# Performance work log

Hardware: AMD Instinct MI355X
Metric: run time of the kernel (lower is better)

The kernel has to match this reference:

```python
import jax, jax.numpy as jnp
import numpy as np

N_NODES = 50000
N_EDGES = 800000
N_GRAPHS = 500
NEG_SLOPE = 0.2
BN_EPS = 1e-5


def gat_layer(x, src, dst, W, al, ar, b):
    # x: [N, F_in]; W: [F_in, H*D]; al/ar: [H, D]; b: [H*D]
    H, D = al.shape
    feat = (x @ W).reshape(N_NODES, H, D)          # [N,H,D]
    el = jnp.sum(feat * al, axis=-1)               # [N,H] src-side score
    er = jnp.sum(feat * ar, axis=-1)               # [N,H] dst-side score
    e = el[src] + er[dst]                          # [E,H]
    e = jnp.where(e > 0, e, NEG_SLOPE * e)         # leaky_relu(0.2)
    # edge softmax over incoming edges of each dst node
    m = jax.ops.segment_max(e, dst, num_segments=N_NODES)       # [N,H]
    ex = jnp.exp(e - m[dst])                                    # [E,H]
    denom = jax.ops.segment_sum(ex, dst, num_segments=N_NODES)  # [N,H]
    alpha = ex / denom[dst]                                     # [E,H]
    # weighted scatter-aggregation of source features
    msg = feat[src] * alpha[:, :, None]                          # [E,H,D]
    out = jax.ops.segment_sum(msg, dst, num_segments=N_NODES)    # [N,H,D]
    return out + b.reshape(H, D)


def batch_norm(x, gamma, beta):
    # training-mode BN over node dimension (biased variance, as torch)
    mu = jnp.mean(x, axis=0)
    var = jnp.mean((x - mu) ** 2, axis=0)
    return gamma * (x - mu) * jax.lax.rsqrt(var + BN_EPS) + beta


def setup_inputs() -> dict:
    key = jax.random.key(0)
    ks = jax.random.split(key, 20)
    s = lambda shape, k, scale=0.05: jax.random.normal(ks[k], shape, jnp.float32) * scale
    return {
        "x": jax.random.normal(ks[0], (N_NODES, 128), jnp.float32),
        "edge_src": jax.random.randint(ks[1], (N_EDGES,), 0, N_NODES),
        "edge_dst": jax.random.randint(ks[2], (N_EDGES,), 0, N_NODES),
        "graph_ids": jax.random.randint(ks[3], (N_NODES,), 0, N_GRAPHS),
        "W0": s((128, 128), 4), "al0": s((4, 32), 5), "ar0": s((4, 32), 6), "b0": jnp.zeros((128,), jnp.float32),
        "W1": s((128, 128), 7), "al1": s((4, 32), 8), "ar1": s((4, 32), 9), "b1": jnp.zeros((128,), jnp.float32),
        "W2": s((128, 32), 10), "al2": s((1, 32), 11), "ar2": s((1, 32), 12), "b2": jnp.zeros((32,), jnp.float32),
        "g0": jnp.ones((128,), jnp.float32), "beta0": jnp.zeros((128,), jnp.float32),
        "g1": jnp.ones((128,), jnp.float32), "beta1": jnp.zeros((128,), jnp.float32),
        "Wc": s((32, 10), 13), "bc": jnp.zeros((10,), jnp.float32),
    }


def reference(x, edge_src, edge_dst, graph_ids,
              W0, al0, ar0, b0, W1, al1, ar1, b1, W2, al2, ar2, b2,
              g0, beta0, g1, beta1, Wc, bc):
    # layer 0: GAT -> flatten heads -> BN -> ReLU (dropout = identity in eval)
    h = gat_layer(x, edge_src, edge_dst, W0, al0, ar0, b0).reshape(N_NODES, -1)
    h = jax.nn.relu(batch_norm(h, g0, beta0))
    # layer 1
    h = gat_layer(h, edge_src, edge_dst, W1, al1, ar1, b1).reshape(N_NODES, -1)
    h = jax.nn.relu(batch_norm(h, g1, beta1))
    # layer 2 (single head) -> squeeze head dim
    h = gat_layer(h, edge_src, edge_dst, W2, al2, ar2, b2)[:, 0, :]  # [N, 32]
    # sum pooling per graph
    hg = jax.ops.segment_sum(h, graph_ids, num_segments=N_GRAPHS)    # [G, 32]
    return hg @ Wc + bc                                              # [G, 10]
```

## Files before the change

kernel.cpp:

```cpp
#include <hip/hip_runtime.h>
#include <math.h>

#define NNODES 50000
#define NEDGES 800000
#define NGRAPHS 500
#define NEG_SLOPE 0.2f
#define BN_EPS 1e-5f
#define NRANGE 196
#define RH_EPB 4096
#define RH_NB ((NEDGES + RH_EPB - 1) / RH_EPB)
#define MAXRE 5120
#define BN_NB 200
#define BN_RPB 250

typedef unsigned int uint;
typedef unsigned short ushort;
typedef __attribute__((ext_vector_type(8))) short bf16x8;
typedef __attribute__((ext_vector_type(4))) float f32x4;

__device__ __forceinline__ float bf2f(ushort u) { return __uint_as_float(((uint)u) << 16); }
__device__ __forceinline__ float bflo(uint u)   { return __uint_as_float(u << 16); }
__device__ __forceinline__ float bfhi(uint u)   { return __uint_as_float(u & 0xffff0000u); }
__device__ __forceinline__ ushort f2bf(float f) {
    uint u = __float_as_uint(f);
    u = (u + 0x7fffu + ((u >> 16) & 1u)) >> 16;
    return (ushort)u;
}

__device__ __forceinline__ float ld_dev(const float* p) {
    return __hip_atomic_load(p, __ATOMIC_RELAXED, __HIP_MEMORY_SCOPE_AGENT);
}
__device__ __forceinline__ void st_dev(float* p, float v) {
    __hip_atomic_store(p, v, __ATOMIC_RELAXED, __HIP_MEMORY_SCOPE_AGENT);
}

__global__ __launch_bounds__(256) void prep_hist_kernel(
        const float* __restrict__ W0, const float* __restrict__ W1,
        const float* __restrict__ W2, ushort* __restrict__ Wt0,
        ushort* __restrict__ Wt1, ushort* __restrict__ Wt2,
        const int* __restrict__ dst, int* __restrict__ rhist,
        int* __restrict__ rowptr) {
    int t = blockIdx.x * 256 + threadIdx.x;
    if (t == 0) rowptr[NNODES] = NEDGES;
    if (t < 16384) {
        int k = t >> 7, m = t & 127;
        Wt0[m * 128 + k] = f2bf(W0[t]);
    } else if (t < 32768) {
        int i = t - 16384;
        int k = i >> 7, m = i & 127;
        Wt1[m * 128 + k] = f2bf(W1[i]);
    } else if (t < 36864) {
        int i = t - 32768;
        int k = i >> 5, m = i & 31;
        Wt2[m * 128 + k] = f2bf(W2[i]);
    }
    __shared__ int cnt[NRANGE];
    for (int i = threadIdx.x; i < NRANGE; i += 256) cnt[i] = 0;
    __syncthreads();
    int base = blockIdx.x * RH_EPB;
    int end = base + RH_EPB; if (end > NEDGES) end = NEDGES;
    for (int i = base + threadIdx.x; i < end; i += 256) atomicAdd(&cnt[dst[i] >> 8], 1);
    __syncthreads();
    for (int i = threadIdx.x; i < NRANGE; i += 256)
        if (cnt[i]) atomicAdd(&rhist[i], cnt[i]);
}

__global__ __launch_bounds__(256) void reorder_kernel(
        const int* __restrict__ src, const int* __restrict__ dst,
        const int* __restrict__ rhist, int* __restrict__ rcursor,
        uint* __restrict__ bucket) {
    __shared__ int cnt[NRANGE];
    __shared__ int bofs[NRANGE];
    __shared__ int rb[256];
    const int t = threadIdx.x;
    rb[t] = (t < NRANGE) ? rhist[t] : 0;
    if (t < NRANGE) cnt[t] = 0;
    __syncthreads();
    for (int off = 1; off < 256; off <<= 1) {
        int u = (t >= off) ? rb[t - off] : 0;
        __syncthreads();
        rb[t] += u;
        __syncthreads();
    }
    int base = blockIdx.x * RH_EPB;
    int end = base + RH_EPB; if (end > NEDGES) end = NEDGES;
    for (int i = base + t; i < end; i += 256) atomicAdd(&cnt[dst[i] >> 8], 1);
    __syncthreads();
    for (int i = t; i < NRANGE; i += 256) {
        int c = cnt[i];
        int ex = (i == 0) ? 0 : rb[i - 1];
        bofs[i] = c ? (ex + atomicAdd(&rcursor[i], c)) : 0;
    }
    __syncthreads();
    for (int i = t; i < NRANGE; i += 256) cnt[i] = 0;
    __syncthreads();
    for (int i = base + t; i < end; i += 256) {
        int d = dst[i], r = d >> 8;
        int loc = atomicAdd(&cnt[r], 1);
        bucket[bofs[r] + loc] = (uint)src[i] | ((uint)(d & 255) << 16);
    }
}

__global__ __launch_bounds__(256) void range_csr_kernel(const int* __restrict__ rhist,
                                                        const uint* __restrict__ bucket,
                                                        int* __restrict__ rowptr,
                                                        int* __restrict__ csr_src) {
    __shared__ uint ebuf[MAXRE];
    __shared__ int deg[256], excl[256], cur[256];
    __shared__ int rb[256];
    const int r = blockIdx.x;
    const int t = threadIdx.x;
    rb[t] = (t < NRANGE) ? rhist[t] : 0;
    __syncthreads();
    for (int off = 1; off < 256; off <<= 1) {
        int u = (t >= off) ? rb[t - off] : 0;
        __syncthreads();
        rb[t] += u;
        __syncthreads();
    }
    const int b0 = (r == 0) ? 0 : rb[r - 1];
    const int cnt = rb[r] - b0;
    deg[t] = 0; cur[t] = 0;
    __syncthreads();
    for (int i = t; i < cnt; i += 256) {
        uint e = bucket[b0 + i];
        ebuf[i] = e;
        atomicAdd(&deg[e >> 16], 1);
    }
    __syncthreads();
    excl[t] = deg[t];
    __syncthreads();
    for (int off = 1; off < 256; off <<= 1) {
        int u = (t >= off) ? excl[t - off] : 0;
        __syncthreads();
        excl[t] += u;
        __syncthreads();
    }
    int myExcl = (t == 0) ? 0 : excl[t - 1];
    __syncthreads();
    excl[t] = myExcl;
    __syncthreads();
    int node = r * 256 + t;
    if (node < NNODES) rowptr[node] = b0 + myExcl;
    for (int i = t; i < cnt; i += 256) {
        uint e = ebuf[i];
        int dl = e >> 16;
        int loc = atomicAdd(&cur[dl], 1);
        csr_src[b0 + excl[dl] + loc] = (int)(e & 0xffffu);
    }
}

template <int M, bool HASBN>
__global__ __launch_bounds__(256) void gemm_mfma_kernel(
        const void* __restrict__ Xv, const ushort* __restrict__ Wt,
        const float* __restrict__ scale, const float* __restrict__ shift,
        const float* __restrict__ al, const float* __restrict__ ar,
        ushort* __restrict__ Y, float* __restrict__ el, float* __restrict__ er, int N) {
    constexpr int H   = M / 32;
    constexpr int BR  = (M == 128) ? 64 : 128;
    constexpr int RT  = (M == 128) ? 4 : 2;
    constexpr int CT  = 2;
    constexpr int LDK = 136;
    __shared__ ushort xs[BR][LDK];
    __shared__ ushort ws[M][LDK];
    __shared__ float scs[128], shs[128];

    const int tid = threadIdx.x, wv = tid >> 6, lane = tid & 63;
    const int rowBase = blockIdx.x * BR;

    if (HASBN) {
        if (tid < 128) {
            scs[tid] = scale[tid];
            shs[tid] = shift[tid];
        }
        __syncthreads();
    }

    if (HASBN) {
        const ushort* X = (const ushort*)Xv;
        for (int i = tid; i < BR * 16; i += 256) {
            int rr = i >> 4, q = i & 15;
            int gr = rowBase + rr;
            uint4 u = make_uint4(0, 0, 0, 0);
            if (gr < N) u = *(const uint4*)(X + (size_t)gr * 128 + q * 8);
            uint arr[4] = {u.x, u.y, u.z, u.w};
            ushort* o = &xs[rr][q * 8];
#pragma unroll
            for (int j = 0; j < 4; ++j) {
                int c = q * 8 + j * 2;
                float lo = fmaxf(bflo(arr[j]) * scs[c] + shs[c], 0.f);
                float hi = fmaxf(bfhi(arr[j]) * scs[c + 1] + shs[c + 1], 0.f);
                o[j * 2]     = f2bf(lo);
                o[j * 2 + 1] = f2bf(hi);
            }
        }
    } else {
        const float* X = (const float*)Xv;
        for (int i = tid; i < BR * 32; i += 256) {
            int rr = i >> 5, c4 = i & 31;
            int gr = rowBase + rr;
            float4 v = make_float4(0.f, 0.f, 0.f, 0.f);
            if (gr < N) v = *(const float4*)(X + (size_t)gr * 128 + c4 * 4);
            ushort* o = &xs[rr][c4 * 4];
            o[0] = f2bf(v.x); o[1] = f2bf(v.y); o[2] = f2bf(v.z); o[3] = f2bf(v.w);
        }
    }
    for (int i = tid; i < M * 16; i += 256) {
        int rr = i >> 4, kc = (i & 15) * 8;
        *(uint4*)&ws[rr][kc] = *(const uint4*)(Wt + rr * 128 + kc);
    }
    __syncthreads();

    const int waveRow = (M == 128) ? 0 : (wv * 32);
    const int waveCol = (M == 128) ? (wv * 32) : 0;
    const int fr = lane & 15, quad = lane >> 4;

    f32x4 acc[RT][CT];
#pragma unroll
    for (int rt = 0; rt < RT; ++rt)
#pragma unroll
        for (int ct = 0; ct < CT; ++ct) acc[rt][ct] = (f32x4){0.f, 0.f, 0.f, 0.f};

#pragma unroll
    for (int ks = 0; ks < 4; ++ks) {
        const int kb = ks * 32 + quad * 8;
        bf16x8 a[RT], b[CT];
#pragma unroll
        for (int rt = 0; rt < RT; ++rt) a[rt] = *(const bf16x8*)&xs[waveRow + rt * 16 + fr][kb];
#pragma unroll
        for (int ct = 0; ct < CT; ++ct) b[ct] = *(const bf16x8*)&ws[waveCol + ct * 16 + fr][kb];
#pragma unroll
        for (int rt = 0; rt < RT; ++rt)
#pragma unroll
            for (int ct = 0; ct < CT; ++ct)
                acc[rt][ct] = __builtin_amdgcn_mfma_f32_16x16x32_bf16(a[rt], b[ct], acc[rt][ct], 0, 0, 0);
    }

#pragma unroll
    for (int rt = 0; rt < RT; ++rt)
#pragma unroll
        for (int ct = 0; ct < CT; ++ct)
#pragma unroll
            for (int rg = 0; rg < 4; ++rg) {
                int gr = rowBase + waveRow + rt * 16 + quad * 4 + rg;
                int gc = waveCol + ct * 16 + fr;
                if (gr < N) Y[(size_t)gr * M + gc] = f2bf(acc[rt][ct][rg]);
            }

    const float a0 = al[waveCol + fr],      a1 = al[waveCol + 16 + fr];
    const float g0 = ar[waveCol + fr],      g1 = ar[waveCol + 16 + fr];
    const int h = (M == 128) ? wv : 0;
#pragma unroll
    for (int rt = 0; rt < RT; ++rt)
#pragma unroll
        for (int rg = 0; rg < 4; ++rg) {
            float pe = acc[rt][0][rg] * a0 + acc[rt][1][rg] * a1;
            float pr = acc[rt][0][rg] * g0 + acc[rt][1][rg] * g1;
#pragma unroll
            for (int off = 1; off < 16; off <<= 1) {
                pe += __shfl_xor(pe, off);
                pr += __shfl_xor(pr, off);
            }
            int grow = rowBase + waveRow + rt * 16 + quad * 4 + rg;
            if (fr == 0 && grow < N) {
                el[grow * H + h] = pe;
                er[grow * H + h] = pr;
            }
        }
}

__global__ __launch_bounds__(256) void gat_gather4_kernel(
        const int* __restrict__ rowptr, const int* __restrict__ csr_src,
        const float* __restrict__ el, const float* __restrict__ er,
        const ushort* __restrict__ feat, const float* __restrict__ bias,
        ushort* __restrict__ xnext) {
    const int d = __builtin_amdgcn_readfirstlane(
        (int)((blockIdx.x * blockDim.x + threadIdx.x) >> 6));
    const int lane = threadIdx.x & 63;
    if (d >= NNODES) return;
    const int h   = lane >> 4;
    const int k   = lane & 15;
    const int grp = lane & 48;
    const int c0  = lane * 2;
    const int r0 = rowptr[d];
    const int deg = rowptr[d + 1] - r0;
    const float erh = er[d * 4 + h];
    float dnm = 0.f, ax = 0.f, ay = 0.f;

    for (int j0 = 0; j0 < deg; j0 += 16) {
        int eidx = j0 + k;
        int s_e = 0;
        float ex = 0.f;
        if (eidx < deg) {
            s_e = csr_src[r0 + eidx];
            float v = el[s_e * 4 + h] + erh;
            v = v > 0.f ? v : NEG_SLOPE * v;
            ex = __expf(v);
        }
        dnm += ex;
        uint u[16];
#pragma unroll
        for (int jj = 0; jj < 16; ++jj) {
            int sj = __builtin_amdgcn_readlane(s_e, jj);
            u[jj] = *(const uint*)(feat + (size_t)sj * 128 + c0);
        }
#pragma unroll
        for (int jj = 0; jj < 16; ++jj) {
            float exj = __shfl(ex, grp + jj);
            ax = fmaf(exj, bflo(u[jj]), ax);
            ay = fmaf(exj, bfhi(u[jj]), ay);
        }
    }
#pragma unroll
    for (int off = 1; off < 16; off <<= 1) dnm += __shfl_xor(dnm, off);
    float inv = (dnm > 0.f) ? 1.f / dnm : 0.f;
    float vx = ax * inv + bias[c0];
    float vy = ay * inv + bias[c0 + 1];
    uint pk = ((uint)f2bf(vy) << 16) | (uint)f2bf(vx);
    *(uint*)(xnext + (size_t)d * 128 + c0) = pk;
}

__global__ __launch_bounds__(256) void bn_stats_kernel(
        const ushort* __restrict__ X, float* __restrict__ psum, float* __restrict__ psumsq,
        const float* __restrict__ g, const float* __restrict__ beta,
        float* __restrict__ scale, float* __restrict__ shift, int* __restrict__ counter) {
    const uint* X32 = (const uint*)X;
    int uc = threadIdx.x & 63;
    int rq = threadIdx.x >> 6;
    int r0 = blockIdx.x * BN_RPB;
    float s0 = 0.f, s1 = 0.f, ss0 = 0.f, ss1 = 0.f;
    for (int r = r0 + rq; r < r0 + BN_RPB; r += 4) {
        uint u = X32[(size_t)r * 64 + uc];
        float lo = bflo(u), hi = bfhi(u);
        s0 += lo; ss0 += lo * lo;
        s1 += hi; ss1 += hi * hi;
    }
    __shared__ float red[4][256], redsq[4][256];
    red[rq][uc * 2] = s0;      red[rq][uc * 2 + 1] = s1;
    redsq[rq][uc * 2] = ss0;   redsq[rq][uc * 2 + 1] = ss1;
    __syncthreads();
    int t = threadIdx.x;
    if (t < 128) {
        st_dev(&psum[blockIdx.x * 128 + t], red[0][t] + red[1][t] + red[2][t] + red[3][t]);
    } else {
        int c = t - 128;
        st_dev(&psumsq[blockIdx.x * 128 + c], redsq[0][c] + redsq[1][c] + redsq[2][c] + redsq[3][c]);
    }
    __syncthreads();
    __shared__ int isLast;
    if (t == 0) isLast = (atomicAdd(counter, 1) == (int)gridDim.x - 1);
    __syncthreads();
    if (!isLast) return;
    __threadfence();
    if (t < 128) {
        float s = 0.f, ss = 0.f;
        for (int b = 0; b < BN_NB; ++b) {
            s += ld_dev(&psum[b * 128 + t]);
            ss += ld_dev(&psumsq[b * 128 + t]);
        }
        const float inv = 1.f / NNODES;
        float mu = s * inv;
        float var = ss * inv - mu * mu;
        float sc = g[t] * rsqrtf(var + BN_EPS);
        scale[t] = sc;
        shift[t] = beta[t] - mu * sc;
    }
}

__global__ __launch_bounds__(256) void gat_gather1_kernel(
        const int* __restrict__ rowptr, const int* __restrict__ csr_src,
        const float* __restrict__ el, const float* __restrict__ er,
        const ushort* __restrict__ feat, const float* __restrict__ bias,
        const int* __restrict__ gid, float* __restrict__ pooled) {
    const int d = __builtin_amdgcn_readfirstlane(
        (int)((blockIdx.x * blockDim.x + threadIdx.x) >> 6));
    int lane = threadIdx.x & 63;
    if (d >= NNODES) return;
    const int r0 = rowptr[d];
    const int deg = rowptr[d + 1] - r0;
    const int half = lane >> 5;
    const int c    = lane & 31;
    const float erh = er[d];
    float dnm = 0.f, acc = 0.f;

    for (int j0 = 0; j0 < deg; j0 += 32) {
        int eidx = j0 + (lane & 31);
        int s_e = 0;
        float ex = 0.f;
        if (eidx < deg) {
            s_e = csr_src[r0 + eidx];
            float v = el[s_e] + erh;
            v = v > 0.f ? v : NEG_SLOPE * v;
            ex = __expf(v);
        }
        dnm += ex;
        ushort u[16];
#pragma unroll
        for (int jj = 0; jj < 16; ++jj) {
            int sj = __shfl(s_e, 2 * jj + half);
            u[jj] = feat[(size_t)sj * 32 + c];
        }
#pragma unroll
        for (int jj = 0; jj < 16; ++jj) {
            float exj = __shfl(ex, 2 * jj + half);
            acc = fmaf(exj, bf2f(u[jj]), acc);
        }
    }
#pragma unroll
    for (int off = 1; off < 32; off <<= 1) dnm += __shfl_xor(dnm, off);
    acc += __shfl_down(acc, 32);
    if (half == 0) {
        float inv = (dnm > 0.f) ? 1.f / dnm : 0.f;
        atomicAdd(&pooled[gid[d] * 32 + c], acc * inv + bias[c]);
    }
}

__global__ void classify_kernel(const float* __restrict__ pooled, const float* __restrict__ Wc,
                                const float* __restrict__ bc, float* __restrict__ out) {
    int t = blockIdx.x * blockDim.x + threadIdx.x;
    if (t >= NGRAPHS * 10) return;
    int gIdx = t / 10, j = t % 10;
    float s = bc[j];
#pragma unroll
    for (int c = 0; c < 32; ++c) s += pooled[gIdx * 32 + c] * Wc[c * 10 + j];
    out[t] = s;
}

extern "C" void kernel_launch(void* const* d_in, const int* in_sizes, int n_in,
                              void* d_out, int out_size, void* d_ws, size_t ws_size,
                              hipStream_t stream) {
    const float* x     = (const float*)d_in[0];
    const int*   esrc  = (const int*)d_in[1];
    const int*   edst  = (const int*)d_in[2];
    const int*   gid   = (const int*)d_in[3];
    const float* W0    = (const float*)d_in[4];
    const float* al0   = (const float*)d_in[5];
    const float* ar0   = (const float*)d_in[6];
    const float* b0    = (const float*)d_in[7];
    const float* W1    = (const float*)d_in[8];
    const float* al1   = (const float*)d_in[9];
    const float* ar1   = (const float*)d_in[10];
    const float* b1    = (const float*)d_in[11];
    const float* W2    = (const float*)d_in[12];
    const float* al2   = (const float*)d_in[13];
    const float* ar2   = (const float*)d_in[14];
    const float* b2    = (const float*)d_in[15];
    const float* g0    = (const float*)d_in[16];
    const float* beta0 = (const float*)d_in[17];
    const float* g1    = (const float*)d_in[18];
    const float* beta1 = (const float*)d_in[19];
    const float* Wc    = (const float*)d_in[20];
    const float* bc    = (const float*)d_in[21];

    int*   counters = (int*)d_ws;
    int*   rhist    = counters + 8;
    int*   rcursor  = rhist + NRANGE;
    float* pooled   = (float*)(rcursor + NRANGE);
    float* psum     = pooled + NGRAPHS * 32;
    float* psumsq   = psum + BN_NB * 128;
    float* scale0   = psumsq + BN_NB * 128;
    float* shift0   = scale0 + 128;
    float* scale1   = shift0 + 128;
    float* shift1   = scale1 + 128;
    int*   rowptr   = (int*)(shift1 + 128);
    int*   csr_src  = rowptr + NNODES + 1;
    uint*  bucket   = (uint*)(csr_src + NEDGES);
    size_t ofs = (size_t)((int*)(bucket + NEDGES) - (int*)d_ws);
    ofs = (ofs + 3) & ~(size_t)3;
    ushort* featbf = (ushort*)((int*)d_ws + ofs);
    ushort* xnext  = featbf + (size_t)NNODES * 128;
    float*  el     = (float*)(xnext + (size_t)NNODES * 128);
    float*  er     = el + (size_t)NNODES * 4;
    ushort* Wt0    = (ushort*)(er + (size_t)NNODES * 4);
    ushort* Wt1    = Wt0 + 128 * 128;
    ushort* Wt2    = Wt1 + 128 * 128;

    const int T = 256;
    float* out = (float*)d_out;

    hipMemsetAsync(counters, 0, (size_t)(8 + NRANGE + NRANGE + NGRAPHS * 32) * 4, stream);
    prep_hist_kernel<<<RH_NB, T, 0, stream>>>(W0, W1, W2, Wt0, Wt1, Wt2, edst, rhist, rowptr);

    reorder_kernel<<<RH_NB, T, 0, stream>>>(esrc, edst, rhist, rcursor, bucket);
    range_csr_kernel<<<NRANGE, T, 0, stream>>>(rhist, bucket, rowptr, csr_src);

    const int GATHER_BLOCKS  = (NNODES * 64) / T;
    const int GEMM128_BLOCKS = (NNODES + 63) / 64;
    const int GEMM32_BLOCKS  = (NNODES + 127) / 128;

    gemm_mfma_kernel<128, false><<<GEMM128_BLOCKS, T, 0, stream>>>(
        x, Wt0, nullptr, nullptr, al0, ar0, featbf, el, er, NNODES);
    gat_gather4_kernel<<<GATHER_BLOCKS, T, 0, stream>>>(rowptr, csr_src, el, er, featbf, b0, xnext);
    bn_stats_kernel<<<BN_NB, T, 0, stream>>>(xnext, psum, psumsq, g0, beta0, scale0, shift0,
                                             &counters[0]);

    gemm_mfma_kernel<128, true><<<GEMM128_BLOCKS, T, 0, stream>>>(
        xnext, Wt1, scale0, shift0, al1, ar1, featbf, el, er, NNODES);
    gat_gather4_kernel<<<GATHER_BLOCKS, T, 0, stream>>>(rowptr, csr_src, el, er, featbf, b1, xnext);
    bn_stats_kernel<<<BN_NB, T, 0, stream>>>(xnext, psum, psumsq, g1, beta1, scale1, shift1,
                                             &counters[1]);

    gemm_mfma_kernel<32, true><<<GEMM32_BLOCKS, T, 0, stream>>>(
        xnext, Wt2, scale1, shift1, al2, ar2, featbf, el, er, NNODES);
    gat_gather1_kernel<<<GATHER_BLOCKS, T, 0, stream>>>(rowptr, csr_src, el, er, featbf, b2,
                                                        gid, pooled);

    classify_kernel<<<(NGRAPHS * 10 + T - 1) / T, T, 0, stream>>>(pooled, Wc, bc, out);
}
```

Measured before the change: 358.4 us.

## Prefetch next edge chunk in gather, stage GEMM output via LDS, retune block sizes

Result: no change. 356.0 us (-0.7%).

```diff
diff --git a/kernel.cpp b/kernel.cpp
--- a/kernel.cpp
+++ b/kernel.cpp
@@ -7,11 +7,11 @@
 #define NEG_SLOPE 0.2f
 #define BN_EPS 1e-5f
 #define NRANGE 196
-#define RH_EPB 4096
+#define RH_EPB 2048
 #define RH_NB ((NEDGES + RH_EPB - 1) / RH_EPB)
 #define MAXRE 5120
-#define BN_NB 200
-#define BN_RPB 250
+#define BN_NB 400
+#define BN_RPB 125
 
 typedef unsigned int uint;
 typedef unsigned short ushort;
@@ -162,7 +162,6 @@
     constexpr int CT  = 2;
     constexpr int LDK = 136;
     __shared__ ushort xs[BR][LDK];
-    __shared__ ushort ws[M][LDK];
     __shared__ float scs[128], shs[128];
 
     const int tid = threadIdx.x, wv = tid >> 6, lane = tid & 63;
@@ -205,10 +204,6 @@
             o[0] = f2bf(v.x); o[1] = f2bf(v.y); o[2] = f2bf(v.z); o[3] = f2bf(v.w);
         }
     }
-    for (int i = tid; i < M * 16; i += 256) {
-        int rr = i >> 4, kc = (i & 15) * 8;
-        *(uint4*)&ws[rr][kc] = *(const uint4*)(Wt + rr * 128 + kc);
-    }
     __syncthreads();
 
     const int waveRow = (M == 128) ? 0 : (wv * 32);
@@ -228,24 +223,14 @@
 #pragma unroll
         for (int rt = 0; rt < RT; ++rt) a[rt] = *(const bf16x8*)&xs[waveRow + rt * 16 + fr][kb];
 #pragma unroll
-        for (int ct = 0; ct < CT; ++ct) b[ct] = *(const bf16x8*)&ws[waveCol + ct * 16 + fr][kb];
+        for (int ct = 0; ct < CT; ++ct)
+            b[ct] = *(const bf16x8*)(Wt + (size_t)(waveCol + ct * 16 + fr) * 128 + kb);
 #pragma unroll
         for (int rt = 0; rt < RT; ++rt)
 #pragma unroll
             for (int ct = 0; ct < CT; ++ct)
                 acc[rt][ct] = __builtin_amdgcn_mfma_f32_16x16x32_bf16(a[rt], b[ct], acc[rt][ct], 0, 0, 0);
     }
-
-#pragma unroll
-    for (int rt = 0; rt < RT; ++rt)
-#pragma unroll
-        for (int ct = 0; ct < CT; ++ct)
-#pragma unroll
-            for (int rg = 0; rg < 4; ++rg) {
-                int gr = rowBase + waveRow + rt * 16 + quad * 4 + rg;
-                int gc = waveCol + ct * 16 + fr;
-                if (gr < N) Y[(size_t)gr * M + gc] = f2bf(acc[rt][ct][rg]);
-            }
 
     const float a0 = al[waveCol + fr],      a1 = al[waveCol + 16 + fr];
     const float g0 = ar[waveCol + fr],      g1 = ar[waveCol + 16 + fr];
@@ -267,6 +252,40 @@
                 er[grow * H + h] = pr;
             }
         }
+
+    __syncthreads();
+#pragma unroll
+    for (int rt = 0; rt < RT; ++rt)
+#pragma unroll
+        for (int ct = 0; ct < CT; ++ct)
+#pragma unroll
+            for (int rg = 0; rg < 4; ++rg) {
+                int lr = waveRow + rt * 16 + quad * 4 + rg;
+                int lc = waveCol + ct * 16 + fr;
+                xs[lr][lc] = f2bf(acc[rt][ct][rg]);
+            }
+    __syncthreads();
+    if (M == 128) {
+        int row = tid >> 2, seg = tid & 3;
+        int gr = rowBase + row;
+        if (gr < N) {
+#pragma unroll
+            for (int q = 0; q < 4; ++q) {
+                int col = (seg * 4 + q) * 8;
+                *(uint4*)(Y + (size_t)gr * 128 + col) = *(const uint4*)&xs[row][col];
+            }
+        }
+    } else {
+        int row = tid >> 1, hf = tid & 1;
+        int gr = rowBase + row;
+        if (gr < N) {
+#pragma unroll
+            for (int q = 0; q < 2; ++q) {
+                int col = (hf * 2 + q) * 8;
+                *(uint4*)(Y + (size_t)gr * 32 + col) = *(const uint4*)&xs[row][col];
+            }
+        }
+    }
 }
 
 __global__ __launch_bounds__(256) void gat_gather4_kernel(
@@ -287,29 +306,37 @@
     const float erh = er[d * 4 + h];
     float dnm = 0.f, ax = 0.f, ay = 0.f;
 
+    int s_c = 0; float ex_c = 0.f;
+    if (k < deg) {
+        s_c = csr_src[r0 + k];
+        float v = el[s_c * 4 + h] + erh;
+        v = v > 0.f ? v : NEG_SLOPE * v;
+        ex_c = __expf(v);
+    }
     for (int j0 = 0; j0 < deg; j0 += 16) {
-        int eidx = j0 + k;
-        int s_e = 0;
-        float ex = 0.f;
-        if (eidx < deg) {
-            s_e = csr_src[r0 + eidx];
-            float v = el[s_e * 4 + h] + erh;
+        const int nidx = j0 + 16 + k;
+        int s_n = 0;
+        if (nidx < deg) s_n = csr_src[r0 + nidx];
+        dnm += ex_c;
+        uint u[16];
+#pragma unroll
+        for (int jj = 0; jj < 16; ++jj) {
+            int sj = __builtin_amdgcn_readlane(s_c, jj);
+            u[jj] = *(const uint*)(feat + (size_t)sj * 128 + c0);
+        }
+        float ex_n = 0.f;
+        if (nidx < deg) {
+            float v = el[s_n * 4 + h] + erh;
             v = v > 0.f ? v : NEG_SLOPE * v;
-            ex = __expf(v);
-        }
-        dnm += ex;
-        uint u[16];
+            ex_n = __expf(v);
+        }
 #pragma unroll
         for (int jj = 0; jj < 16; ++jj) {
-            int sj = __builtin_amdgcn_readlane(s_e, jj);
-            u[jj] = *(const uint*)(feat + (size_t)sj * 128 + c0);
-        }
-#pragma unroll
-        for (int jj = 0; jj < 16; ++jj) {
-            float exj = __shfl(ex, grp + jj);
+            float exj = __shfl(ex_c, grp + jj);
             ax = fmaf(exj, bflo(u[jj]), ax);
             ay = fmaf(exj, bfhi(u[jj]), ay);
         }
+        s_c = s_n; ex_c = ex_n;
     }
 #pragma unroll
     for (int off = 1; off < 16; off <<= 1) dnm += __shfl_xor(dnm, off);
```
